# Kernel tuning notes

Hardware: AMD Instinct MI355X
Metric: run time of the kernel (lower is better)

## Reference

```python
import jax, jax.numpy as jnp
import numpy as np

N = 50000
E_RAND = 800000
F_IN = 128
HID = 128
HEADS = 8
LAYERS = 2
DH = HID // HEADS  # 16


def setup_inputs() -> dict:
    key = jax.random.key(0)
    ks = jax.random.split(key, 8)
    x = jax.random.normal(ks[0], (N, F_IN), dtype=jnp.float32)
    # random edges + self loops so every row of the segment-softmax is nonempty
    rnd = jax.random.randint(ks[1], (2, E_RAND), 0, N, dtype=jnp.int32)
    loops = jnp.tile(jnp.arange(N, dtype=jnp.int32), (2, 1))
    edge_idx = jnp.concatenate([rnd, loops], axis=1)  # [2, 850000]
    edge_vals = jnp.ones((edge_idx.shape[1],), dtype=jnp.float32)
    # glorot-style params
    enc_W = jax.random.normal(ks[2], (F_IN, HID), dtype=jnp.float32) * np.sqrt(2.0 / (F_IN + HID))
    enc_b = jnp.zeros((HID,), dtype=jnp.float32)
    W_stack = jax.random.normal(ks[3], (LAYERS, HEADS, HID, DH), dtype=jnp.float32) * np.sqrt(2.0 / (HID + DH))
    a_stack = jax.random.normal(ks[4], (LAYERS, HEADS, 2 * DH), dtype=jnp.float32) * np.sqrt(2.0 / (1 + 2 * DH))
    return {"x": x, "edge_idx": edge_idx, "edge_vals": edge_vals,
            "enc_W": enc_W, "enc_b": enc_b, "W_stack": W_stack, "a_stack": a_stack}


def _gat_layer(xin, row, col, edge_vals, W, a):
    # xin: [N, HID]; W: [H, HID, DH]; a: [H, 2*DH]
    n = xin.shape[0]
    h = jnp.einsum('nd,hdf->hnf', xin, W)            # [H, N, DH]
    a_src, a_dst = a[:, :DH], a[:, DH:]
    alpha_src = jnp.einsum('hnf,hf->hn', h, a_src)   # a . h[row] part
    alpha_dst = jnp.einsum('hnf,hf->hn', h, a_dst)   # a . h[col] part
    logits = edge_vals[None, :] * (alpha_src[:, row] + alpha_dst[:, col])  # [H, E]
    e = jnp.exp(jax.nn.leaky_relu(logits, 0.2))      # unnormalized attention
    rowsum = jax.ops.segment_sum(e.T, row, num_segments=n)               # [N, H]
    msg = e[:, :, None] * h[:, col, :]               # [H, E, DH]
    agg = jax.vmap(lambda m: jax.ops.segment_sum(m, row, num_segments=n))(msg)  # [H, N, DH]
    out = agg / rowsum.T[:, :, None]
    return jnp.transpose(out, (1, 0, 2)).reshape(n, -1)  # concat heads -> [N, HID]


def reference(x, edge_idx, edge_vals, enc_W, enc_b, W_stack, a_stack):
    row, col = edge_idx[0], edge_idx[1]
    xc = x @ enc_W + enc_b  # encoder
    L = W_stack.shape[0]
    for ell in range(L):
        out = _gat_layer(xc, row, col, edge_vals, W_stack[ell], a_stack[ell])
        if ell != L - 1:
            out = jax.nn.elu(out)  # feat_drop is identity in eval mode
        xc = out + xc if ell > 0 else out  # use_residual=True
    # single snapshot: stack over T=1 then permute(1,0,2) -> [N, 1, HID]
    return xc[:, None, :]
```

## Files before the change

### kernel.cpp

```cpp
#include <hip/hip_runtime.h>
#include <hip/hip_bf16.h>


typedef __attribute__((ext_vector_type(8))) short short8;
typedef __attribute__((ext_vector_type(4))) float floatx4;
typedef __attribute__((ext_vector_type(2))) float floatx2;

__device__ __forceinline__ unsigned f2u(float f) { return __float_as_uint(f); }
__device__ __forceinline__ float u2f(unsigned u) { return __uint_as_float(u); }
__device__ __forceinline__ unsigned short f2bf_rne(float x) {
    unsigned u = f2u(x);
    unsigned r = (u + 0x7FFF + ((u >> 16) & 1)) >> 16;
    return (unsigned short)r;
}


__global__ void histpack_kernel(const int* __restrict__ row, int* __restrict__ deg,
                                int* __restrict__ rank, int E, int EB,
                                const float* __restrict__ encW,
                                const float* __restrict__ Wstack,
                                short8* __restrict__ Wh, short8* __restrict__ Wl) {
    int b = blockIdx.x;
    if (b < EB) {
        int e = b * 256 + threadIdx.x;
        if (e < E) rank[e] = atomicAdd(&deg[row[e]], 1);
        return;
    }
    int idx = (b - EB) * 256 + threadIdx.x;
    if (idx >= 3 * 2048) return;
    int mat = idx >> 11;
    int r = idx & 2047;
    int lane = r & 63;
    int tile = r >> 6;
    int ct = tile >> 2, kt = tile & 3;
    int ncol = ct * 16 + (lane & 15);
    int k0 = kt * 32 + ((lane >> 4) * 8);
    short8 hv, lv;
#pragma unroll
    for (int j = 0; j < 8; ++j) {
        int k = k0 + j;
        float w = (mat == 0)
            ? encW[k * 128 + ncol]
            : Wstack[(mat - 1) * 16384 + (ncol >> 4) * 2048 + k * 16 + (ncol & 15)];
        unsigned u = f2u(w);
        hv[j] = (short)(u >> 16);
        float hf = u2f(u & 0xFFFF0000u);
        float l = w - hf;
        lv[j] = (short)(f2u(l) >> 16);
    }
    Wh[idx] = hv;
    Wl[idx] = lv;
}

__global__ void gathercv_kernel(const int* __restrict__ perm, const int* __restrict__ colv,
                                const float* __restrict__ ev, int2* __restrict__ csr_cv,
                                int E) {
    int s = blockIdx.x * 256 + threadIdx.x;
    if (s < E) {
        int e = perm[s];
        csr_cv[s] = make_int2(colv[e], __float_as_int(ev[e]));
    }
}


__device__ __forceinline__ void
gemm_body(int bid, const float* __restrict__ A, const short8* __restrict__ Bh,
          const short8* __restrict__ Bl, const float* __restrict__ bias,
          const float* __restrict__ avec, float* __restrict__ Cf,
          unsigned short* __restrict__ Cbf,
          float* __restrict__ asrc, float* __restrict__ adst, int n, int flags) {
    int wave = threadIdx.x >> 6;
    int lane = threadIdx.x & 63;
    int q = lane >> 4;
    int col = lane & 15;
    int n0w = bid * 64 + wave * 16;

    int arow = min(n0w + col, n - 1);
    const float* Arow = A + (size_t)arow * 128;
    int kb = q * 8;
    short8 Ah[4], Al[4];
#pragma unroll
    for (int kt = 0; kt < 4; ++kt) {
        float4 f0 = *(const float4*)(Arow + kt * 32 + kb);
        float4 f1 = *(const float4*)(Arow + kt * 32 + kb + 4);
        float fv[8] = {f0.x, f0.y, f0.z, f0.w, f1.x, f1.y, f1.z, f1.w};
#pragma unroll
        for (int j = 0; j < 8; ++j) {
            unsigned u = f2u(fv[j]);
            Ah[kt][j] = (short)(u >> 16);
            float hf = u2f(u & 0xFFFF0000u);
            float l = fv[j] - hf;
            Al[kt][j] = (short)(f2u(l) >> 16);
        }
    }

    int nbase = n0w + q * 4;
#pragma unroll
    for (int ct = 0; ct < 8; ++ct) {
        short8 bh[4], bl[4];
#pragma unroll
        for (int kt = 0; kt < 4; ++kt) {
            bh[kt] = Bh[(ct * 4 + kt) * 64 + lane];
            bl[kt] = Bl[(ct * 4 + kt) * 64 + lane];
        }
        float bv = (flags & 1) ? bias[ct * 16 + col] : 0.f;
        floatx4 acc = {bv, bv, bv, bv};
#pragma unroll
        for (int kt = 0; kt < 4; ++kt) {
            acc = __builtin_amdgcn_mfma_f32_16x16x32_bf16(Ah[kt], bh[kt], acc, 0, 0, 0);
            acc = __builtin_amdgcn_mfma_f32_16x16x32_bf16(Al[kt], bh[kt], acc, 0, 0, 0);
            acc = __builtin_amdgcn_mfma_f32_16x16x32_bf16(Ah[kt], bl[kt], acc, 0, 0, 0);
        }
#pragma unroll
        for (int reg = 0; reg < 4; ++reg) {
            int node = nbase + reg;
            if (node < n) {
                if (flags & 4) Cbf[(size_t)node * 128 + ct * 16 + col] = f2bf_rne(acc[reg]);
                else           Cf[(size_t)node * 128 + ct * 16 + col] = acc[reg];
            }
        }
        if (flags & 2) {
            float a_s = avec[ct * 32 + col];
            float a_d = avec[ct * 32 + 16 + col];
#pragma unroll
            for (int reg = 0; reg < 4; ++reg) {
                float ps = acc[reg] * a_s;
                float pd = acc[reg] * a_d;
#pragma unroll
                for (int off = 8; off; off >>= 1) {
                    ps += __shfl_down(ps, off, 16);
                    pd += __shfl_down(pd, off, 16);
                }
                int node = nbase + reg;
                if (col == 0 && node < n) {
                    asrc[node * 8 + ct] = ps;
                    adst[node * 8 + ct] = pd;
                }
            }
        }
    }
}

__global__ __launch_bounds__(256) void
gemm_mfma(const float* __restrict__ A, const short8* __restrict__ Bh,
          const short8* __restrict__ Bl, const float* __restrict__ avec,
          unsigned short* __restrict__ Cbf,
          float* __restrict__ asrc, float* __restrict__ adst, int n) {
    gemm_body(blockIdx.x, A, Bh, Bl, nullptr, avec, nullptr, Cbf, asrc, adst, n, 2 | 4);
}

__global__ __launch_bounds__(256) void
enc_scan_kernel(const float* __restrict__ x, const short8* __restrict__ Wh,
                const short8* __restrict__ Wl, const float* __restrict__ encb,
                float* __restrict__ xc, int n, int GBn,
                const int* __restrict__ deg, int* __restrict__ rowstart,
                int* __restrict__ gcursor) {
    __shared__ int sd[256];
    __shared__ int sbase;
    if ((int)blockIdx.x < GBn) {
        gemm_body(blockIdx.x, x, Wh, Wl, encb, nullptr, xc, nullptr, nullptr, nullptr, n, 1);
        return;
    }
    int t = threadIdx.x;
    int idx = (blockIdx.x - GBn) * 256 + t;
    int v = (idx < n) ? deg[idx] : 0;
    sd[t] = v;
    __syncthreads();
    for (int off = 1; off < 256; off <<= 1) {
        int add = (t >= off) ? sd[t - off] : 0;
        __syncthreads();
        sd[t] += add;
        __syncthreads();
    }
    if (t == 255) sbase = atomicAdd(gcursor, sd[255]);
    __syncthreads();
    if (idx < n) rowstart[idx] = sbase + sd[t] - v;
}

__global__ __launch_bounds__(256) void
sperm_gemm_kernel(const float* __restrict__ xc, const short8* __restrict__ Wh1,
                  const short8* __restrict__ Wl1, const float* __restrict__ avec,
                  unsigned short* __restrict__ hbf, float* __restrict__ asrc,
                  float* __restrict__ adst, int n, int GBn,
                  const int* __restrict__ row, const int* __restrict__ rank,
                  const int* __restrict__ rowstart, int* __restrict__ perm, int E) {
    if ((int)blockIdx.x < GBn) {
        gemm_body(blockIdx.x, xc, Wh1, Wl1, nullptr, avec, nullptr, hbf, asrc, adst, n, 2 | 4);
        return;
    }
    int e = (blockIdx.x - GBn) * 256 + threadIdx.x;
    if (e < E) perm[rowstart[row[e]] + rank[e]] = e;
}


__global__ __launch_bounds__(256) void
aggregate_kernel(const int* __restrict__ rowstart, const int* __restrict__ degv,
                 const int2* __restrict__ cv,
                 const unsigned short* __restrict__ hbf,
                 const float* __restrict__ asrc, const float* __restrict__ adst,
                 const float* __restrict__ resid, float* __restrict__ out,
                 int mode, int n) {
    int wid = (blockIdx.x * 256 + threadIdx.x) >> 6;
    if (wid >= n) return;
    int lane = threadIdx.x & 63;
    int grp = lane >> 4;
    int l4 = lane & 15;
    int h = l4 >> 1;

    int s = rowstart[wid];
    int e = s + degv[wid];
    float as_w = asrc[wid * 8 + h];

    floatx2 acc0 = {0.f, 0.f}, acc1 = {0.f, 0.f};
    floatx2 acc2 = {0.f, 0.f}, acc3 = {0.f, 0.f};
    float ws = 0.f;

#pragma unroll 4
    for (int j = s + grp; j < e; j += 4) {
        int2 cvj = cv[j];
        int c = cvj.x;
        float v = __int_as_float(cvj.y);
        float lg = v * (as_w + adst[c * 8 + h]);
        float lr = fmaxf(lg, 0.2f * lg);
        float w = __expf(lr);
        uint4 hv = *(const uint4*)(hbf + (size_t)c * 128 + l4 * 8);
        floatx2 w2 = {w, w};
        floatx2 p0 = {u2f(hv.x << 16), u2f(hv.x & 0xFFFF0000u)};
        floatx2 p1 = {u2f(hv.y << 16), u2f(hv.y & 0xFFFF0000u)};
        floatx2 p2 = {u2f(hv.z << 16), u2f(hv.z & 0xFFFF0000u)};
        floatx2 p3 = {u2f(hv.w << 16), u2f(hv.w & 0xFFFF0000u)};
        acc0 += w2 * p0;
        acc1 += w2 * p1;
        acc2 += w2 * p2;
        acc3 += w2 * p3;
        ws += w;
    }

    float a0 = acc0.x, a1 = acc0.y, a2 = acc1.x, a3 = acc1.y;
    float a4 = acc2.x, a5 = acc2.y, a6 = acc3.x, a7 = acc3.y;

#define RED4(x) x += __shfl_xor(x, 16); x += __shfl_xor(x, 32);
    RED4(a0) RED4(a1) RED4(a2) RED4(a3)
    RED4(a4) RED4(a5) RED4(a6) RED4(a7)
    RED4(ws)
#undef RED4

    if (grp == 0) {
        float inv = 1.0f / ws;
        float o[8] = {a0 * inv, a1 * inv, a2 * inv, a3 * inv,
                      a4 * inv, a5 * inv, a6 * inv, a7 * inv};
        size_t base = (size_t)wid * 128 + l4 * 8;
        if (mode == 0) {
#pragma unroll
            for (int k = 0; k < 8; ++k) o[k] = o[k] > 0.f ? o[k] : expm1f(o[k]);
        } else {
            float4 r0 = *(const float4*)(resid + base);
            float4 r1 = *(const float4*)(resid + base + 4);
            o[0] += r0.x; o[1] += r0.y; o[2] += r0.z; o[3] += r0.w;
            o[4] += r1.x; o[5] += r1.y; o[6] += r1.z; o[7] += r1.w;
        }
        float4 w0 = {o[0], o[1], o[2], o[3]};
        float4 w1 = {o[4], o[5], o[6], o[7]};
        *(float4*)(out + base) = w0;
        *(float4*)(out + base + 4) = w1;
    }
}


extern "C" void kernel_launch(void* const* d_in, const int* in_sizes, int n_in,
                              void* d_out, int out_size, void* d_ws, size_t ws_size,
                              hipStream_t stream) {
    const int N = in_sizes[0] / 128;
    const int E = in_sizes[2];

    const float* x      = (const float*)d_in[0];
    const int*   eidx   = (const int*)d_in[1];
    const float* ev     = (const float*)d_in[2];
    const float* encW   = (const float*)d_in[3];
    const float* encb   = (const float*)d_in[4];
    const float* Wstack = (const float*)d_in[5];
    const float* astack = (const float*)d_in[6];
    float* out = (float*)d_out;

    const int* row = eidx;
    const int* colv = eidx + E;

    char* p = (char*)d_ws;
    float* xc   = (float*)p; p += (size_t)N * 128 * 4;
    float* xcB  = (float*)p; p += (size_t)N * 128 * 4;
    unsigned short* hbf = (unsigned short*)p; p += (size_t)N * 128 * 2;
    float* asrc = (float*)p; p += (size_t)N * 8 * 4;
    float* adst = (float*)p; p += (size_t)N * 8 * 4;
    short8* Wh  = (short8*)p; p += 3 * 2048 * 16;
    short8* Wl  = (short8*)p; p += 3 * 2048 * 16;
    int2* csr_cv = (int2*)p; p += (size_t)E * 8;
    int* rowstart = (int*)p; p += (size_t)N * 4;
    int* deg    = (int*)p;   p += (size_t)N * 4;
    int* gcursor = (int*)p;  p += 4;

    int* rank = (int*)xcB;
    int* perm = rank + E;

    const int NB256 = (N + 255) / 256;
    const int GB = (N + 63) / 64;
    const int AGG = (N + 3) / 4;
    const int EB = (E + 255) / 256;

    hipMemsetAsync(deg, 0, (size_t)(N + 1) * 4, stream);
    histpack_kernel<<<EB + 24, 256, 0, stream>>>(row, deg, rank, E, EB,
                                                 encW, Wstack, Wh, Wl);

    enc_scan_kernel<<<GB + NB256, 256, 0, stream>>>(x, Wh, Wl, encb, xc, N, GB,
                                                    deg, rowstart, gcursor);

    sperm_gemm_kernel<<<GB + EB, 256, 0, stream>>>(xc, Wh + 2048, Wl + 2048, astack,
                                                   hbf, asrc, adst, N, GB,
                                                   row, rank, rowstart, perm, E);

    gathercv_kernel<<<EB, 256, 0, stream>>>(perm, colv, ev, csr_cv, E);

    aggregate_kernel<<<AGG, 256, 0, stream>>>(rowstart, deg, csr_cv, hbf, asrc, adst,
                                              nullptr, xcB, 0, N);

    gemm_mfma<<<GB, 256, 0, stream>>>(xcB, Wh + 4096, Wl + 4096, astack + 256,
                                      hbf, asrc, adst, N);
    aggregate_kernel<<<AGG, 256, 0, stream>>>(rowstart, deg, csr_cv, hbf, asrc, adst,
                                              xcB, out, 1, N);
}
```

Baseline: 301.7 us.

## Stage GEMM weights in LDS and make row-pointer scan deterministic via chunk histograms

```diff
diff --git a/kernel.cpp b/kernel.cpp
--- a/kernel.cpp
+++ b/kernel.cpp
@@ -16,14 +16,25 @@
 
 
 __global__ void histpack_kernel(const int* __restrict__ row, int* __restrict__ deg,
-                                int* __restrict__ rank, int E, int EB,
+                                int* __restrict__ chunkdeg, int* __restrict__ rank,
+                                int E, int EB, int NCH,
                                 const float* __restrict__ encW,
                                 const float* __restrict__ Wstack,
                                 short8* __restrict__ Wh, short8* __restrict__ Wl) {
     int b = blockIdx.x;
     if (b < EB) {
-        int e = b * 256 + threadIdx.x;
-        if (e < E) rank[e] = atomicAdd(&deg[row[e]], 1);
+        __shared__ int ch[256];
+        int t = threadIdx.x;
+        ch[t] = 0;
+        __syncthreads();
+        int e = b * 256 + t;
+        if (e < E) {
+            int r = row[e];
+            rank[e] = atomicAdd(&deg[r], 1);
+            atomicAdd(&ch[r >> 8], 1);
+        }
+        __syncthreads();
+        if (t < NCH && ch[t] > 0) atomicAdd(&chunkdeg[t], ch[t]);
         return;
     }
     int idx = (b - EB) * 256 + threadIdx.x;
@@ -69,6 +80,13 @@
           const float* __restrict__ avec, float* __restrict__ Cf,
           unsigned short* __restrict__ Cbf,
           float* __restrict__ asrc, float* __restrict__ adst, int n, int flags) {
+    __shared__ short8 lb[4096];
+    int t = threadIdx.x;
+#pragma unroll
+    for (int i = 0; i < 8; ++i) lb[i * 256 + t] = Bh[i * 256 + t];
+#pragma unroll
+    for (int i = 0; i < 8; ++i) lb[2048 + i * 256 + t] = Bl[i * 256 + t];
+
     int wave = threadIdx.x >> 6;
     int lane = threadIdx.x & 63;
     int q = lane >> 4;
@@ -93,6 +111,7 @@
             Al[kt][j] = (short)(f2u(l) >> 16);
         }
     }
+    __syncthreads();
 
     int nbase = n0w + q * 4;
 #pragma unroll
@@ -100,8 +119,8 @@
         short8 bh[4], bl[4];
 #pragma unroll
         for (int kt = 0; kt < 4; ++kt) {
-            bh[kt] = Bh[(ct * 4 + kt) * 64 + lane];
-            bl[kt] = Bl[(ct * 4 + kt) * 64 + lane];
+            bh[kt] = lb[(ct * 4 + kt) * 64 + lane];
+            bl[kt] = lb[2048 + (ct * 4 + kt) * 64 + lane];
         }
         float bv = (flags & 1) ? bias[ct * 16 + col] : 0.f;
         floatx4 acc = {bv, bv, bv, bv};
@@ -153,16 +172,27 @@
 enc_scan_kernel(const float* __restrict__ x, const short8* __restrict__ Wh,
                 const short8* __restrict__ Wl, const float* __restrict__ encb,
                 float* __restrict__ xc, int n, int GBn,
-                const int* __restrict__ deg, int* __restrict__ rowstart,
-                int* __restrict__ gcursor) {
-    __shared__ int sd[256];
-    __shared__ int sbase;
+                const int* __restrict__ deg, const int* __restrict__ chunkdeg,
+                int* __restrict__ rowptr) {
     if ((int)blockIdx.x < GBn) {
         gemm_body(blockIdx.x, x, Wh, Wl, encb, nullptr, xc, nullptr, nullptr, nullptr, n, 1);
         return;
     }
+    __shared__ int sd[256];
+    __shared__ int sbase;
     int t = threadIdx.x;
-    int idx = (blockIdx.x - GBn) * 256 + t;
+    int cb = blockIdx.x - GBn;
+    int acc = 0;
+    for (int k = t; k < cb; k += 256) acc += chunkdeg[k];
+    sd[t] = acc;
+    __syncthreads();
+    for (int off = 128; off; off >>= 1) {
+        if (t < off) sd[t] += sd[t + off];
+        __syncthreads();
+    }
+    if (t == 0) sbase = sd[0];
+    __syncthreads();
+    int idx = cb * 256 + t;
     int v = (idx < n) ? deg[idx] : 0;
     sd[t] = v;
     __syncthreads();
@@ -172,9 +202,8 @@
         sd[t] += add;
         __syncthreads();
     }
-    if (t == 255) sbase = atomicAdd(gcursor, sd[255]);
-    __syncthreads();
-    if (idx < n) rowstart[idx] = sbase + sd[t] - v;
+    if (idx < n) rowptr[idx] = sbase + sd[t] - v;
+    if (idx == n - 1) rowptr[n] = sbase + sd[t];
 }
 
 __global__ __launch_bounds__(256) void
@@ -183,19 +212,18 @@
                   unsigned short* __restrict__ hbf, float* __restrict__ asrc,
                   float* __restrict__ adst, int n, int GBn,
                   const int* __restrict__ row, const int* __restrict__ rank,
-                  const int* __restrict__ rowstart, int* __restrict__ perm, int E) {
+                  const int* __restrict__ rowptr, int* __restrict__ perm, int E) {
     if ((int)blockIdx.x < GBn) {
         gemm_body(blockIdx.x, xc, Wh1, Wl1, nullptr, avec, nullptr, hbf, asrc, adst, n, 2 | 4);
         return;
     }
     int e = (blockIdx.x - GBn) * 256 + threadIdx.x;
-    if (e < E) perm[rowstart[row[e]] + rank[e]] = e;
+    if (e < E) perm[rowptr[row[e]] + rank[e]] = e;
 }
 
 
 __global__ __launch_bounds__(256) void
-aggregate_kernel(const int* __restrict__ rowstart, const int* __restrict__ degv,
-                 const int2* __restrict__ cv,
+aggregate_kernel(const int* __restrict__ rowptr, const int2* __restrict__ cv,
                  const unsigned short* __restrict__ hbf,
                  const float* __restrict__ asrc, const float* __restrict__ adst,
                  const float* __restrict__ resid, float* __restrict__ out,
@@ -207,8 +235,8 @@
     int l4 = lane & 15;
     int h = l4 >> 1;
 
-    int s = rowstart[wid];
-    int e = s + degv[wid];
+    int s = rowptr[wid];
+    int e = rowptr[wid + 1];
     float as_w = asrc[wid * 8 + h];
 
     floatx2 acc0 = {0.f, 0.f}, acc1 = {0.f, 0.f};
@@ -285,6 +313,8 @@
     const int* row = eidx;
     const int* colv = eidx + E;
 
+    const int NCH = (N + 255) / 256;
+
     char* p = (char*)d_ws;
     float* xc   = (float*)p; p += (size_t)N * 128 * 4;
     float* xcB  = (float*)p; p += (size_t)N * 128 * 4;
@@ -294,36 +324,35 @@
     short8* Wh  = (short8*)p; p += 3 * 2048 * 16;
     short8* Wl  = (short8*)p; p += 3 * 2048 * 16;
     int2* csr_cv = (int2*)p; p += (size_t)E * 8;
-    int* rowstart = (int*)p; p += (size_t)N * 4;
+    int* rowptr = (int*)p;   p += (size_t)(N + 1) * 4;
     int* deg    = (int*)p;   p += (size_t)N * 4;
-    int* gcursor = (int*)p;  p += 4;
+    int* chunkdeg = (int*)p; p += (size_t)NCH * 4;
 
     int* rank = (int*)xcB;
     int* perm = rank + E;
 
-    const int NB256 = (N + 255) / 256;
     const int GB = (N + 63) / 64;
     const int AGG = (N + 3) / 4;
     const int EB = (E + 255) / 256;
 
-    hipMemsetAsync(deg, 0, (size_t)(N + 1) * 4, stream);
-    histpack_kernel<<<EB + 24, 256, 0, stream>>>(row, deg, rank, E, EB,
+    hipMemsetAsync(deg, 0, (size_t)(N + NCH) * 4, stream);
+    histpack_kernel<<<EB + 24, 256, 0, stream>>>(row, deg, chunkdeg, rank, E, EB, NCH,
                                                  encW, Wstack, Wh, Wl);
 
-    enc_scan_kernel<<<GB + NB256, 256, 0, stream>>>(x, Wh, Wl, encb, xc, N, GB,
-                                                    deg, rowstart, gcursor);
+    enc_scan_kernel<<<GB + NCH, 256, 0, stream>>>(x, Wh, Wl, encb, xc, N, GB,
+                                                  deg, chunkdeg, rowptr);
 
     sperm_gemm_kernel<<<GB + EB, 256, 0, stream>>>(xc, Wh + 2048, Wl + 2048, astack,
                                                    hbf, asrc, adst, N, GB,
-                                                   row, rank, rowstart, perm, E);
+                                                   row, rank, rowptr, perm, E);
 
     gathercv_kernel<<<EB, 256, 0, stream>>>(perm, colv, ev, csr_cv, E);
 
-    aggregate_kernel<<<AGG, 256, 0, stream>>>(rowstart, deg, csr_cv, hbf, asrc, adst,
+    aggregate_kernel<<<AGG, 256, 0, stream>>>(rowptr, csr_cv, hbf, asrc, adst,
                                               nullptr, xcB, 0, N);
 
     gemm_mfma<<<GB, 256, 0, stream>>>(xcB, Wh + 4096, Wl + 4096, astack + 256,
                                       hbf, asrc, adst, N);
-    aggregate_kernel<<<AGG, 256, 0, stream>>>(rowstart, deg, csr_cv, hbf, asrc, adst,
+    aggregate_kernel<<<AGG, 256, 0, stream>>>(rowptr, csr_cv, hbf, asrc, adst,
                                               xcB, out, 1, N);
 }
```

Result: slower. 364.9 us (+21.0%).
